# Performance work log

Measured on AMD Instinct MI355X. Metric: run time of the kernel, lower is better.

Reference implementation:

```python
import jax, jax.numpy as jnp
import numpy as np

HIDDEN, N_HEADS, N_KV, HD = 2560, 32, 8, 80
B, S = 2, 2048

def apply_rope(x, cos_f, sin_f):
    # x: [B, S, H, hd]; cos_f/sin_f: [S, hd]
    seq_len = x.shape[1]
    cos = cos_f[:seq_len][None, :, None, :]
    sin = sin_f[:seq_len][None, :, None, :]
    hd = x.shape[-1]
    x1, x2 = x[..., : hd // 2], x[..., hd // 2 :]
    return x * cos + jnp.concatenate([-x2, x1], axis=-1) * sin


def setup_inputs() -> dict:
    key = jax.random.key(0)
    ks = jax.random.split(key, 7)
    sd = 0.02
    return {
        "x": jax.random.normal(ks[0], (B, S, HIDDEN), dtype=jnp.float32),
        "cos_f": jax.random.uniform(ks[1], (S, HD), dtype=jnp.float32),
        "sin_f": jax.random.uniform(ks[2], (S, HD), dtype=jnp.float32),
        "Wq": jax.random.normal(ks[3], (HIDDEN, N_HEADS * HD), dtype=jnp.float32) * sd,
        "Wk": jax.random.normal(ks[4], (HIDDEN, N_KV * HD), dtype=jnp.float32) * sd,
        "Wv": jax.random.normal(ks[5], (HIDDEN, N_KV * HD), dtype=jnp.float32) * sd,
        "Wo": jax.random.normal(ks[6], (N_HEADS * HD, HIDDEN), dtype=jnp.float32) * sd,
    }


def reference(x, cos_f, sin_f, Wq, Wk, Wv, Wo):
    b, s, _ = x.shape
    q = (x @ Wq).reshape(b, s, N_HEADS, HD)
    k = (x @ Wk).reshape(b, s, N_KV, HD)
    v = (x @ Wv).reshape(b, s, N_KV, HD)
    q = apply_rope(q, cos_f, sin_f)
    k = apply_rope(k, cos_f, sin_f)
    g = N_HEADS // N_KV
    k = jnp.repeat(k, g, axis=2)  # [b, s, n_heads, hd]
    v = jnp.repeat(v, g, axis=2)
    q, k, v = [jnp.transpose(t, (0, 2, 1, 3)) for t in (q, k, v)]  # [b, h, s, hd]
    scale = jnp.sqrt(jnp.float32(HD))
    w = jnp.einsum("bhqd,bhkd->bhqk", q, k) / scale
    causal = jnp.triu(jnp.full((s, s), -1e9, dtype=w.dtype), k=1)
    w = w + causal[None, None]
    w = jax.nn.softmax(w.astype(jnp.float32), axis=-1).astype(q.dtype)
    o = jnp.einsum("bhqk,bhkd->bhqd", w, v)
    o = jnp.transpose(o, (0, 2, 1, 3)).reshape(b, s, N_HEADS * HD)
    return o @ Wo
```

## Files before the change

### kernel.cpp

```cpp
#include <hip/hip_runtime.h>
#include <hip/hip_bf16.h>
#include <math.h>

#define HIDDEN 2560
#define NH 32
#define NKV 8
#define HD 80
#define BATCH 2
#define SEQ 2048
#define QH_COLS (NH*HD)
#define KV_COLS (NKV*HD)
#define ROWS (BATCH*SEQ)

typedef __attribute__((ext_vector_type(4))) float floatx4;
typedef __attribute__((ext_vector_type(16))) float floatx16;
typedef __attribute__((ext_vector_type(8))) short shortx8;
typedef __attribute__((ext_vector_type(4))) unsigned short u16x4;
typedef unsigned short u16;

__device__ inline u16 f2bf(float f) { __hip_bfloat16 h = __float2bfloat16(f); return *(u16*)&h; }
__device__ inline int swz(int r) { return (r + (r >> 2)) & 3; }
__device__ inline void storeC(float v, float* p) { *p = v; }
__device__ inline void storeC(float v, u16* p) { *p = f2bf(v); }

#if __has_builtin(__builtin_amdgcn_exp2f)
__device__ inline float fexp2(float x) { return __builtin_amdgcn_exp2f(x); }
#else
__device__ inline float fexp2(float x) { return __expf(x * 0.6931471805599453f); }
#endif

__device__ __forceinline__ unsigned cvtpk(float lo, float hi2) {
    unsigned r;
    asm("v_cvt_pk_bf16_f32 %0, %1, %2" : "=v"(r) : "v"(lo), "v"(hi2));
    return r;
}
__device__ __forceinline__ void pl32swap(unsigned &a, unsigned &b) {
#if __has_builtin(__builtin_amdgcn_permlane32_swap)
    auto r = __builtin_amdgcn_permlane32_swap(a, b, false, false);
    a = r[0]; b = r[1];
#else
    asm("v_permlane32_swap_b32 %0, %1" : "+v"(a), "+v"(b));
#endif
}

__global__ __launch_bounds__(256) void conv_bf16(const float* __restrict__ x,
                                                 u16* __restrict__ y) {
    int i = (blockIdx.x * 256 + threadIdx.x) * 4;
    float4 v = *(const float4*)(x + i);
    u16x4 o = { f2bf(v.x), f2bf(v.y), f2bf(v.z), f2bf(v.w) };
    *(u16x4*)(y + i) = o;
}

__global__ __launch_bounds__(256) void transpose_conv(const float* __restrict__ W,
                                                      u16* __restrict__ Wt,
                                                      int K, int N) {
    __shared__ float tile[64][65];
    const int tid = threadIdx.x;
    const int n0 = blockIdx.x * 64, k0 = blockIdx.y * 64;
    const int r = tid >> 4, c4 = (tid & 15) * 4;
#pragma unroll
    for (int i = 0; i < 4; i++) {
        float4 v = *(const float4*)(W + (size_t)(k0 + r + i * 16) * N + n0 + c4);
        tile[r + i * 16][c4 + 0] = v.x;
        tile[r + i * 16][c4 + 1] = v.y;
        tile[r + i * 16][c4 + 2] = v.z;
        tile[r + i * 16][c4 + 3] = v.w;
    }
    __syncthreads();
    const int n = tid >> 2, kg = (tid & 3) * 16;
    __align__(16) u16 tmp[16];
#pragma unroll
    for (int j = 0; j < 16; j++) tmp[j] = f2bf(tile[kg + j][n]);
    u16* dst = Wt + (size_t)(n0 + n) * K + k0 + kg;
    *(uint4*)dst = *(const uint4*)tmp;
    *(uint4*)(dst + 8) = *(const uint4*)(tmp + 8);
}

template <typename OutT>
__global__ __launch_bounds__(256) void gemm_mfma(const u16* __restrict__ A,
                                                 const u16* __restrict__ Bt,
                                                 OutT* __restrict__ C,
                                                 int M, int N, int K) {
    __shared__ __align__(16) u16 As[128 * 32];
    __shared__ __align__(16) u16 Bs[128 * 32];
    const int tid = threadIdx.x;
    const int wave = tid >> 6, lane = tid & 63;
    const int m16 = lane & 15, quad = lane >> 4;
    const int wr = wave >> 1, wc = wave & 1;
    const int bm = blockIdx.y * 128, bn = blockIdx.x * 128;

    const u16* gA[2]; const u16* gB[2]; u16* lA[2]; u16* lB[2];
#pragma unroll
    for (int i = 0; i < 2; i++) {
        int c = wave + i * 4;
        int o = c * 1024 + lane * 16;
        int r = o >> 6;
        int s = (o >> 4) & 3;
        int kb = s ^ swz(r);
        gA[i] = A  + (size_t)(bm + r) * K + kb * 8;
        gB[i] = Bt + (size_t)(bn + r) * K + kb * 8;
        lA[i] = As + (o >> 1);
        lB[i] = Bs + (o >> 1);
    }
    int offA[4], offB[4];
#pragma unroll
    for (int i = 0; i < 4; i++) {
        int ra = wr * 64 + i * 16 + m16;
        offA[i] = ra * 32 + (quad ^ swz(ra)) * 8;
        int rb = wc * 64 + i * 16 + m16;
        offB[i] = rb * 32 + (quad ^ swz(rb)) * 8;
    }

    floatx4 acc[4][4];
#pragma unroll
    for (int i = 0; i < 4; i++)
#pragma unroll
        for (int j = 0; j < 4; j++) acc[i][j] = (floatx4){0.f, 0.f, 0.f, 0.f};

    for (int k0 = 0; k0 < K; k0 += 32) {
#pragma unroll
        for (int i = 0; i < 2; i++) {
            __builtin_amdgcn_global_load_lds(
                (const __attribute__((address_space(1))) unsigned int*)(gA[i] + k0),
                (__attribute__((address_space(3))) unsigned int*)lA[i], 16, 0, 0);
            __builtin_amdgcn_global_load_lds(
                (const __attribute__((address_space(1))) unsigned int*)(gB[i] + k0),
                (__attribute__((address_space(3))) unsigned int*)lB[i], 16, 0, 0);
        }
        __syncthreads();
        shortx8 af[4], bfr[4];
#pragma unroll
        for (int i = 0; i < 4; i++) af[i] = *(const shortx8*)(As + offA[i]);
#pragma unroll
        for (int j = 0; j < 4; j++) bfr[j] = *(const shortx8*)(Bs + offB[j]);
#pragma unroll
        for (int i = 0; i < 4; i++)
#pragma unroll
            for (int j = 0; j < 4; j++)
                acc[i][j] = __builtin_amdgcn_mfma_f32_16x16x32_bf16(af[i], bfr[j], acc[i][j], 0, 0, 0);
        __syncthreads();
    }
#pragma unroll
    for (int i = 0; i < 4; i++)
#pragma unroll
        for (int j = 0; j < 4; j++)
#pragma unroll
            for (int p = 0; p < 4; p++) {
                int row = bm + wr * 64 + i * 16 + quad * 4 + p;
                int col = bn + wc * 64 + j * 16 + m16;
                storeC(acc[i][j][p], &C[(size_t)row * N + col]);
            }
}

__global__ __launch_bounds__(256) void rope_bf16(__hip_bfloat16* __restrict__ qh,
                                                 __hip_bfloat16* __restrict__ kh,
                                                 const float* __restrict__ cf,
                                                 const float* __restrict__ sf) {
    int idx = blockIdx.x * 256 + threadIdx.x;
    int d  = idx % 40;
    int t  = idx / 40;
    int hh = t % (NH + NKV);
    int g  = t / (NH + NKV);
    int s  = g & (SEQ - 1);
    float c1 = cf[s * HD + d],      s1 = sf[s * HD + d];
    float c2 = cf[s * HD + d + 40], s2 = sf[s * HD + d + 40];
    const float qsc = (hh < NH) ? (float)(0.11180339887498949 * 1.4426950408889634) : 1.0f;
    __hip_bfloat16* p = (hh < NH) ? (qh + (size_t)g * QH_COLS + hh * HD)
                                  : (kh + (size_t)g * KV_COLS + (hh - NH) * HD);
    float x1 = __bfloat162float(p[d]);
    float x2 = __bfloat162float(p[d + 40]);
    p[d]      = __float2bfloat16((x1 * c1 - x2 * s1) * qsc);
    p[d + 40] = __float2bfloat16((x2 * c2 + x1 * s2) * qsc);
}

__device__ __forceinline__ void stage_K(const u16* kg, u16* dst, int wave, int lane) {
#pragma unroll
    for (int t = 0; t < 2; t++) {
        int s = t * 256 + wave * 64 + lane;
        int db = t * 4 + wave;
        __builtin_amdgcn_global_load_lds(
            (const __attribute__((address_space(1))) unsigned int*)(kg + (size_t)lane * KV_COLS + db * 8),
            (__attribute__((address_space(3))) unsigned int*)(dst + s * 8), 16, 0, 0);
    }
    if (wave < 2) {
        int s = 512 + wave * 64 + lane;
        int db = 8 + wave;
        __builtin_amdgcn_global_load_lds(
            (const __attribute__((address_space(1))) unsigned int*)(kg + (size_t)lane * KV_COLS + db * 8),
            (__attribute__((address_space(3))) unsigned int*)(dst + s * 8), 16, 0, 0);
    }
}

__device__ __forceinline__ void load_V(const u16* vg, shortx8* vr, int wave, int lane) {
#pragma unroll
    for (int t = 0; t < 2; t++) {
        int db = t * 4 + wave;
        vr[t] = *(const shortx8*)(vg + (size_t)lane * KV_COLS + db * 8);
    }
    if (wave < 2) vr[2] = *(const shortx8*)(vg + (size_t)lane * KV_COLS + (8 + wave) * 8);
}

__device__ __forceinline__ void scatter_V(u16* Vs, const shortx8* vr, int wave, int lane) {
    const int kc = lane >> 3, jj = lane & 7;
    u16* base = Vs + kc * 768 + jj;
#pragma unroll
    for (int t = 0; t < 2; t++) {
        int db = t * 4 + wave;
#pragma unroll
        for (int i = 0; i < 8; i++) base[db * 64 + ((i ^ kc) << 3)] = vr[t][i];
    }
    if (wave < 2) {
        int db = 8 + wave;
#pragma unroll
        for (int i = 0; i < 8; i++) base[db * 64 + ((i ^ kc) << 3)] = vr[2][i];
    }
}

__global__ __launch_bounds__(256, 3) void attn_mfma(const u16* __restrict__ qg,
                                                    const u16* __restrict__ kgp,
                                                    const u16* __restrict__ vgp,
                                                    u16* __restrict__ ob) {
    __shared__ __align__(16) u16 SM[16384];
    u16* Kbuf = SM;
    u16* Vs   = SM + 10240;

    const int tid  = threadIdx.x;
    const int wave = tid >> 6;
    const int lane = tid & 63;
    const int l31  = lane & 31;
    const int hi   = lane >> 5;

    const int idx = blockIdx.x;
    const int qt  = 15 - (idx >> 6);
    const int hb  = idx & 63;
    const int h   = hb >> 1;
    const int b   = hb & 1;
    const int kvh = h >> 2;
    const int qb  = qt * 128 + wave * 32;

    const u16* qgb = qg + (size_t)(b * SEQ + qt * 128) * QH_COLS + h * HD;
    const u16* kg0 = kgp + (size_t)(b * SEQ) * KV_COLS + kvh * HD;
    const u16* vg0 = vgp + (size_t)(b * SEQ) * KV_COLS + kvh * HD;

    {
        int kc = tid >> 5, o = (tid & 31) * 4;
        *(u16x4*)(Vs + kc * 768 + 640 + o) = (u16x4){0, 0, 0, 0};
    }

#pragma unroll
    for (int t = 0; t < 5; t++) {
        int s = t * 256 + tid;
        int row = s / 10, ch = s % 10;
        __builtin_amdgcn_global_load_lds(
            (const __attribute__((address_space(1))) unsigned int*)(qgb + (size_t)row * QH_COLS + ch * 8),
            (__attribute__((address_space(3))) unsigned int*)(SM + s * 8), 16, 0, 0);
    }
    __syncthreads();
    shortx8 qf[5];
    {
        const u16* qrow = SM + (wave * 32 + l31) * 80 + hi * 8;
#pragma unroll
        for (int c = 0; c < 5; c++) qf[c] = *(const shortx8*)(qrow + c * 16);
    }
    __syncthreads();

    int vbase[4];
#pragma unroll
    for (int c = 0; c < 4; c++) {
        int k8 = c * 2 + hi;
        vbase[c] = k8 * 768 + ((l31 & 24) + ((l31 & 7) ^ k8)) * 8;
    }
    const u16* kfp = Kbuf + hi * 512 + l31 * 8;

    stage_K(kg0, Kbuf, wave, lane);
    shortx8 vr[3];
    load_V(vg0, vr, wave, lane);
    __syncthreads();
    scatter_V(Vs, vr, wave, lane);
    __syncthreads();

    floatx16 Oacc[3];
#pragma unroll
    for (int n = 0; n < 3; n++)
#pragma unroll
        for (int r = 0; r < 16; r++) Oacc[n][r] = 0.0f;
    float mrow = -1.0e30f, lrow = 0.0f;
    int cur = 0;
    const int nkt = 2 * qt + 2;

    for (int kt = 0; kt < nkt; kt++) {
        const bool last = (kt == nkt - 1);
        if (!last) {
            const u16* kg = kg0 + (size_t)(kt + 1) * 64 * KV_COLS;
            const u16* vg = vg0 + (size_t)(kt + 1) * 64 * KV_COLS;
            stage_K(kg, Kbuf + (cur ^ 1) * 5120, wave, lane);
            load_V(vg, vr, wave, lane);
        }

        const bool active = (kt * 64 <= qb + 31);
        if (active) {
            const u16* kp = kfp + cur * 5120;
            const bool kr1   = (kt * 64 + 32 <= qb + 31);
            const bool dmask = (kt * 64 + 63 > qb);
            floatx16 S0, S1;
            {
                floatx16 s;
#pragma unroll
                for (int r = 0; r < 16; r++) s[r] = 0.0f;
#pragma unroll
                for (int c = 0; c < 5; c++) {
                    shortx8 kf = *(const shortx8*)(kp + c * 1024);
                    s = __builtin_amdgcn_mfma_f32_32x32x16_bf16(kf, qf[c], s, 0, 0, 0);
                }
                S0 = s;
            }
            if (kr1) {
                floatx16 s;
#pragma unroll
                for (int r = 0; r < 16; r++) s[r] = 0.0f;
#pragma unroll
                for (int c = 0; c < 5; c++) {
                    shortx8 kf = *(const shortx8*)(kp + c * 1024 + 256);
                    s = __builtin_amdgcn_mfma_f32_32x32x16_bf16(kf, qf[c], s, 0, 0, 0);
                }
                S1 = s;
            }
            const int qrel = qb + l31 - kt * 64;
            if (dmask) {
#pragma unroll
                for (int r = 0; r < 16; r++) {
                    int rr = (r & 3) + 8 * (r >> 2) + 4 * hi;
                    if (rr > qrel) S0[r] = -1.0e30f;
                    if (kr1 && (32 + rr) > qrel) S1[r] = -1.0e30f;
                }
            }
            float mx = mrow;
#pragma unroll
            for (int r = 0; r < 16; r++) mx = fmaxf(mx, S0[r]);
            if (kr1) {
#pragma unroll
                for (int r = 0; r < 16; r++) mx = fmaxf(mx, S1[r]);
            }
            mx = fmaxf(mx, __shfl_xor(mx, 32));
            if (!__all(mx - mrow <= 8.0f)) {
                float alpha = fexp2(mrow - mx);
                lrow *= alpha;
#pragma unroll
                for (int n = 0; n < 3; n++)
#pragma unroll
                    for (int r = 0; r < 16; r++) Oacc[n][r] *= alpha;
                mrow = mx;
            }
            float rsum = 0.0f;
#pragma unroll
            for (int r = 0; r < 16; r++) { float p = fexp2(S0[r] - mrow); rsum += p; S0[r] = p; }
            if (kr1) {
#pragma unroll
                for (int r = 0; r < 16; r++) { float p = fexp2(S1[r] - mrow); rsum += p; S1[r] = p; }
            }
            rsum += __shfl_xor(rsum, 32);
            lrow += rsum;

#pragma unroll
            for (int kr = 0; kr < 2; kr++) {
                if (kr == 1 && !kr1) break;
                floatx16& Sv = (kr == 0) ? S0 : S1;
                unsigned d0[4], d1[4];
#pragma unroll
                for (int m = 0; m < 4; m++) {
                    d0[m] = cvtpk(Sv[4 * m + 0], Sv[4 * m + 1]);
                    d1[m] = cvtpk(Sv[4 * m + 2], Sv[4 * m + 3]);
                }
#pragma unroll
                for (int cb = 0; cb < 2; cb++) {
                    int c = kr * 2 + cb;
                    if (kt * 64 + c * 16 > qb + 31) break;
                    unsigned x0 = d0[2 * cb], y0 = d0[2 * cb + 1];
                    unsigned x1 = d1[2 * cb], y1 = d1[2 * cb + 1];
                    pl32swap(x0, y0);
                    pl32swap(x1, y1);
                    union { unsigned u[4]; shortx8 s8; } pf;
                    pf.u[0] = x0; pf.u[1] = x1; pf.u[2] = y0; pf.u[3] = y1;
#pragma unroll
                    for (int n = 0; n < 3; n++) {
                        shortx8 vf = *(const shortx8*)(Vs + vbase[c] + n * 256);
                        Oacc[n] = __builtin_amdgcn_mfma_f32_32x32x16_bf16(vf, pf.s8, Oacc[n], 0, 0, 0);
                    }
                }
            }
        }

        if (last) break;
        __syncthreads();
        scatter_V(Vs, vr, wave, lane);
        cur ^= 1;
        __syncthreads();
    }

    const float invl = 1.0f / lrow;
    u16* op = ob + (size_t)(b * SEQ + qt * 128 + wave * 32 + l31) * QH_COLS + h * HD + 4 * hi;
#pragma unroll
    for (int n = 0; n < 3; n++) {
        const int mmax = (n == 2) ? 2 : 4;
#pragma unroll
        for (int m = 0; m < mmax; m++) {
            u16x4 o4 = { f2bf(Oacc[n][4 * m + 0] * invl), f2bf(Oacc[n][4 * m + 1] * invl),
                         f2bf(Oacc[n][4 * m + 2] * invl), f2bf(Oacc[n][4 * m + 3] * invl) };
            *(u16x4*)(op + n * 32 + 8 * m) = o4;
        }
    }
}

extern "C" void kernel_launch(void* const* d_in, const int* in_sizes, int n_in,
                              void* d_out, int out_size, void* d_ws, size_t ws_size,
                              hipStream_t stream) {
    const float* x    = (const float*)d_in[0];
    const float* cf   = (const float*)d_in[1];
    const float* sf   = (const float*)d_in[2];
    const float* Wq   = (const float*)d_in[3];
    const float* Wk   = (const float*)d_in[4];
    const float* Wv   = (const float*)d_in[5];
    const float* Wo   = (const float*)d_in[6];
    float* out = (float*)d_out;

    u16* xh  = (u16*)d_ws;
    u16* Wqt = xh  + (size_t)ROWS * QH_COLS;
    u16* Wkt = Wqt + (size_t)QH_COLS * HIDDEN;
    u16* Wvt = Wkt + (size_t)KV_COLS * HIDDEN;
    u16* Wot = Wvt + (size_t)KV_COLS * HIDDEN;
    u16* qh  = Wot + (size_t)HIDDEN * QH_COLS;
    u16* kh  = qh  + (size_t)ROWS * QH_COLS;
    u16* vh  = kh  + (size_t)ROWS * KV_COLS;
    u16* obh = xh;

    dim3 blk(256);
    conv_bf16<<<(ROWS * HIDDEN / 4) / 256, blk, 0, stream>>>(x, xh);
    transpose_conv<<<dim3(QH_COLS / 64, HIDDEN / 64), blk, 0, stream>>>(Wq, Wqt, HIDDEN, QH_COLS);
    transpose_conv<<<dim3(KV_COLS / 64, HIDDEN / 64), blk, 0, stream>>>(Wk, Wkt, HIDDEN, KV_COLS);
    transpose_conv<<<dim3(KV_COLS / 64, HIDDEN / 64), blk, 0, stream>>>(Wv, Wvt, HIDDEN, KV_COLS);
    transpose_conv<<<dim3(HIDDEN / 64, QH_COLS / 64), blk, 0, stream>>>(Wo, Wot, QH_COLS, HIDDEN);

    gemm_mfma<u16><<<dim3(QH_COLS / 128, ROWS / 128), blk, 0, stream>>>(xh, Wqt, qh, ROWS, QH_COLS, HIDDEN);
    gemm_mfma<u16><<<dim3(KV_COLS / 128, ROWS / 128), blk, 0, stream>>>(xh, Wkt, kh, ROWS, KV_COLS, HIDDEN);
    gemm_mfma<u16><<<dim3(KV_COLS / 128, ROWS / 128), blk, 0, stream>>>(xh, Wvt, vh, ROWS, KV_COLS, HIDDEN);

    rope_bf16<<<(ROWS * (NH + NKV) * 40) / 256, blk, 0, stream>>>((__hip_bfloat16*)qh, (__hip_bfloat16*)kh, cf, sf);
    attn_mfma<<<dim3(16 * 64), blk, 0, stream>>>(qh, kh, vh, obh);

    gemm_mfma<float><<<dim3(HIDDEN / 128, ROWS / 128), blk, 0, stream>>>(obh, Wot, out, ROWS, HIDDEN, QH_COLS);
}
```

Baseline: 549.9 us.

## Fuse QKV projections into one GEMM and use 256x256 pipelined MFMA tiles

Concatenates the Wq, Wk and Wv transposed weights so a single GEMM writes an interleaved QKV buffer. RoPE and attention are updated to read it with the wider row stride. The GEMM is replaced with a 512-thread, 256x256-tile kernel with 64-wide K steps, double-buffered global_load_lds prefetch two stages ahead, split barriers and setprio around MFMA bursts. The goal is fewer launches, more data reuse per tile and better overlap of loads with matrix math. The costs are much more LDS per block (128 KB), fewer blocks for the small output projection grid (10x16), and a strided QKV layout for attention loads.

```diff
diff --git a/kernel.cpp b/kernel.cpp
--- a/kernel.cpp
+++ b/kernel.cpp
@@ -10,6 +10,7 @@
 #define SEQ 2048
 #define QH_COLS (NH*HD)
 #define KV_COLS (NKV*HD)
+#define QKV_COLS (QH_COLS + 2*KV_COLS)
 #define ROWS (BATCH*SEQ)
 
 typedef __attribute__((ext_vector_type(4))) float floatx4;
@@ -19,7 +20,6 @@
 typedef unsigned short u16;
 
 __device__ inline u16 f2bf(float f) { __hip_bfloat16 h = __float2bfloat16(f); return *(u16*)&h; }
-__device__ inline int swz(int r) { return (r + (r >> 2)) & 3; }
 __device__ inline void storeC(float v, float* p) { *p = v; }
 __device__ inline void storeC(float v, u16* p) { *p = f2bf(v); }
 
@@ -43,6 +43,10 @@
 #endif
 }
 
+#define GLL(gp, lp) __builtin_amdgcn_global_load_lds( \
+    (const __attribute__((address_space(1))) unsigned int*)(gp), \
+    (__attribute__((address_space(3))) unsigned int*)(lp), 16, 0, 0)
+
 __global__ __launch_bounds__(256) void conv_bf16(const float* __restrict__ x,
                                                  u16* __restrict__ y) {
     int i = (blockIdx.x * 256 + threadIdx.x) * 4;
@@ -77,83 +81,124 @@
 }
 
 template <typename OutT>
-__global__ __launch_bounds__(256) void gemm_mfma(const u16* __restrict__ A,
-                                                 const u16* __restrict__ Bt,
-                                                 OutT* __restrict__ C,
-                                                 int M, int N, int K) {
-    __shared__ __align__(16) u16 As[128 * 32];
-    __shared__ __align__(16) u16 Bs[128 * 32];
+__global__ __launch_bounds__(512, 2) void gemm256(const u16* __restrict__ A,
+                                                  const u16* __restrict__ Bt,
+                                                  OutT* __restrict__ C,
+                                                  int M, int N, int K) {
+    __shared__ __align__(16) u16 SM[65536];
     const int tid = threadIdx.x;
     const int wave = tid >> 6, lane = tid & 63;
     const int m16 = lane & 15, quad = lane >> 4;
-    const int wr = wave >> 1, wc = wave & 1;
-    const int bm = blockIdx.y * 128, bn = blockIdx.x * 128;
-
-    const u16* gA[2]; const u16* gB[2]; u16* lA[2]; u16* lB[2];
-#pragma unroll
-    for (int i = 0; i < 2; i++) {
-        int c = wave + i * 4;
-        int o = c * 1024 + lane * 16;
-        int r = o >> 6;
-        int s = (o >> 4) & 3;
-        int kb = s ^ swz(r);
-        gA[i] = A  + (size_t)(bm + r) * K + kb * 8;
-        gB[i] = Bt + (size_t)(bn + r) * K + kb * 8;
-        lA[i] = As + (o >> 1);
-        lB[i] = Bs + (o >> 1);
-    }
-    int offA[4], offB[4];
-#pragma unroll
-    for (int i = 0; i < 4; i++) {
-        int ra = wr * 64 + i * 16 + m16;
-        offA[i] = ra * 32 + (quad ^ swz(ra)) * 8;
-        int rb = wc * 64 + i * 16 + m16;
-        offB[i] = rb * 32 + (quad ^ swz(rb)) * 8;
-    }
-
-    floatx4 acc[4][4];
-#pragma unroll
-    for (int i = 0; i < 4; i++)
+    const int wm = wave >> 2, wn = wave & 3;
+    const int bm = blockIdx.y * 256, bn = blockIdx.x * 256;
+
+    const int srow = (wave & 3) * 64 + lane;
+    const int skc  = wave >> 2;
+    const u16* pA = A  + (size_t)(bm + srow) * K + skc * 8;
+    const u16* pB = Bt + (size_t)(bn + srow) * K + skc * 8;
+    u16* lsA = SM + skc * 2048 + (wave & 3) * 512 + lane * 8;
+    u16* lsB = lsA + 32768;
+
+    const int aoff = quad * 2048 + (wm * 128 + m16) * 8;
+    const int boff = quad * 2048 + (wn * 64 + m16) * 8 + 32768;
+
+    floatx4 acc[8][4];
+#pragma unroll
+    for (int i = 0; i < 8; i++)
 #pragma unroll
         for (int j = 0; j < 4; j++) acc[i][j] = (floatx4){0.f, 0.f, 0.f, 0.f};
 
-    for (int k0 = 0; k0 < K; k0 += 32) {
-#pragma unroll
-        for (int i = 0; i < 2; i++) {
-            __builtin_amdgcn_global_load_lds(
-                (const __attribute__((address_space(1))) unsigned int*)(gA[i] + k0),
-                (__attribute__((address_space(3))) unsigned int*)lA[i], 16, 0, 0);
-            __builtin_amdgcn_global_load_lds(
-                (const __attribute__((address_space(1))) unsigned int*)(gB[i] + k0),
-                (__attribute__((address_space(3))) unsigned int*)lB[i], 16, 0, 0);
-        }
-        __syncthreads();
-        shortx8 af[4], bfr[4];
-#pragma unroll
-        for (int i = 0; i < 4; i++) af[i] = *(const shortx8*)(As + offA[i]);
-#pragma unroll
-        for (int j = 0; j < 4; j++) bfr[j] = *(const shortx8*)(Bs + offB[j]);
-#pragma unroll
-        for (int i = 0; i < 4; i++)
-#pragma unroll
-            for (int j = 0; j < 4; j++)
-                acc[i][j] = __builtin_amdgcn_mfma_f32_16x16x32_bf16(af[i], bfr[j], acc[i][j], 0, 0, 0);
-        __syncthreads();
-    }
-#pragma unroll
-    for (int i = 0; i < 4; i++)
+    const int nkt = K >> 6;
+
+#pragma unroll
+    for (int t = 0; t < 2; t++) {
+        const int tb = t * 16384, tc = t * 64;
+        GLL(pA + tc,      lsA + tb);        GLL(pA + tc + 16, lsA + tb + 4096);
+        GLL(pB + tc,      lsB + tb);        GLL(pB + tc + 16, lsB + tb + 4096);
+        GLL(pA + tc + 32, lsA + tb + 8192); GLL(pA + tc + 48, lsA + tb + 12288);
+        GLL(pB + tc + 32, lsB + tb + 8192); GLL(pB + tc + 48, lsB + tb + 12288);
+    }
+    asm volatile("s_waitcnt vmcnt(8)" ::: "memory");
+    __builtin_amdgcn_s_barrier();
+
+    for (int kt = 0; kt < nkt; ++kt) {
+        const int ab = (kt & 1) * 16384;
+        const bool pf = (kt + 2 < nkt);
+        const int pc = (kt + 2) * 64;
+        shortx8 af[8], b0, b1, b2, b3;
+
+#pragma unroll
+        for (int i = 0; i < 8; i++) af[i] = *(const shortx8*)(SM + ab + aoff + i * 128);
+        b0 = *(const shortx8*)(SM + ab + boff);
+        b1 = *(const shortx8*)(SM + ab + boff + 128);
+        if (pf) { GLL(pA + pc, lsA + ab); GLL(pA + pc + 16, lsA + ab + 4096); }
+        __builtin_amdgcn_s_barrier();
+        __builtin_amdgcn_s_setprio(1);
+#pragma unroll
+        for (int i = 0; i < 8; i++) {
+            acc[i][0] = __builtin_amdgcn_mfma_f32_16x16x32_bf16(af[i], b0, acc[i][0], 0, 0, 0);
+            acc[i][1] = __builtin_amdgcn_mfma_f32_16x16x32_bf16(af[i], b1, acc[i][1], 0, 0, 0);
+        }
+        __builtin_amdgcn_s_setprio(0);
+        __builtin_amdgcn_s_barrier();
+
+        b2 = *(const shortx8*)(SM + ab + boff + 256);
+        b3 = *(const shortx8*)(SM + ab + boff + 384);
+        if (pf) { GLL(pB + pc, lsB + ab); GLL(pB + pc + 16, lsB + ab + 4096); }
+        __builtin_amdgcn_s_barrier();
+        __builtin_amdgcn_s_setprio(1);
+#pragma unroll
+        for (int i = 0; i < 8; i++) {
+            acc[i][2] = __builtin_amdgcn_mfma_f32_16x16x32_bf16(af[i], b2, acc[i][2], 0, 0, 0);
+            acc[i][3] = __builtin_amdgcn_mfma_f32_16x16x32_bf16(af[i], b3, acc[i][3], 0, 0, 0);
+        }
+        __builtin_amdgcn_s_setprio(0);
+        __builtin_amdgcn_s_barrier();
+
+#pragma unroll
+        for (int i = 0; i < 8; i++) af[i] = *(const shortx8*)(SM + ab + 8192 + aoff + i * 128);
+        b0 = *(const shortx8*)(SM + ab + 8192 + boff);
+        b1 = *(const shortx8*)(SM + ab + 8192 + boff + 128);
+        if (pf) { GLL(pA + pc + 32, lsA + ab + 8192); GLL(pA + pc + 48, lsA + ab + 12288); }
+        __builtin_amdgcn_s_barrier();
+        __builtin_amdgcn_s_setprio(1);
+#pragma unroll
+        for (int i = 0; i < 8; i++) {
+            acc[i][0] = __builtin_amdgcn_mfma_f32_16x16x32_bf16(af[i], b0, acc[i][0], 0, 0, 0);
+            acc[i][1] = __builtin_amdgcn_mfma_f32_16x16x32_bf16(af[i], b1, acc[i][1], 0, 0, 0);
+        }
+        __builtin_amdgcn_s_setprio(0);
+        __builtin_amdgcn_s_barrier();
+
+        b2 = *(const shortx8*)(SM + ab + 8192 + boff + 256);
+        b3 = *(const shortx8*)(SM + ab + 8192 + boff + 384);
+        if (pf) { GLL(pB + pc + 32, lsB + ab + 8192); GLL(pB + pc + 48, lsB + ab + 12288); }
+        __builtin_amdgcn_s_barrier();
+        __builtin_amdgcn_s_setprio(1);
+#pragma unroll
+        for (int i = 0; i < 8; i++) {
+            acc[i][2] = __builtin_amdgcn_mfma_f32_16x16x32_bf16(af[i], b2, acc[i][2], 0, 0, 0);
+            acc[i][3] = __builtin_amdgcn_mfma_f32_16x16x32_bf16(af[i], b3, acc[i][3], 0, 0, 0);
+        }
+        __builtin_amdgcn_s_setprio(0);
+        if (pf) asm volatile("s_waitcnt vmcnt(8)" ::: "memory");
+        else    asm volatile("s_waitcnt vmcnt(0)" ::: "memory");
+        __builtin_amdgcn_s_barrier();
+    }
+
+#pragma unroll
+    for (int i = 0; i < 8; i++)
 #pragma unroll
         for (int j = 0; j < 4; j++)
 #pragma unroll
             for (int p = 0; p < 4; p++) {
-                int row = bm + wr * 64 + i * 16 + quad * 4 + p;
-                int col = bn + wc * 64 + j * 16 + m16;
+                int row = bm + wm * 128 + i * 16 + quad * 4 + p;
+                int col = bn + wn * 64 + j * 16 + m16;
                 storeC(acc[i][j][p], &C[(size_t)row * N + col]);
             }
 }
 
-__global__ __launch_bounds__(256) void rope_bf16(__hip_bfloat16* __restrict__ qh,
-                                                 __hip_bfloat16* __restrict__ kh,
+__global__ __launch_bounds__(256) void rope_bf16(__hip_bfloat16* __restrict__ qkv,
                                                  const float* __restrict__ cf,
                                                  const float* __restrict__ sf) {
     int idx = blockIdx.x * 256 + threadIdx.x;
@@ -165,8 +210,8 @@
     float c1 = cf[s * HD + d],      s1 = sf[s * HD + d];
     float c2 = cf[s * HD + d + 40], s2 = sf[s * HD + d + 40];
     const float qsc = (hh < NH) ? (float)(0.11180339887498949 * 1.4426950408889634) : 1.0f;
-    __hip_bfloat16* p = (hh < NH) ? (qh + (size_t)g * QH_COLS + hh * HD)
-                                  : (kh + (size_t)g * KV_COLS + (hh - NH) * HD);
+    __hip_bfloat16* p = (hh < NH) ? (qkv + (size_t)g * QKV_COLS + hh * HD)
+                                  : (qkv + (size_t)g * QKV_COLS + QH_COLS + (hh - NH) * HD);
     float x1 = __bfloat162float(p[d]);
     float x2 = __bfloat162float(p[d + 40]);
     p[d]      = __float2bfloat16((x1 * c1 - x2 * s1) * qsc);
@@ -178,16 +223,12 @@
     for (int t = 0; t < 2; t++) {
         int s = t * 256 + wave * 64 + lane;
         int db = t * 4 + wave;
-        __builtin_amdgcn_global_load_lds(
-            (const __attribute__((address_space(1))) unsigned int*)(kg + (size_t)lane * KV_COLS + db * 8),
-            (__attribute__((address_space(3))) unsigned int*)(dst + s * 8), 16, 0, 0);
+        GLL(kg + (size_t)lane * QKV_COLS + db * 8, dst + s * 8);
     }
     if (wave < 2) {
         int s = 512 + wave * 64 + lane;
         int db = 8 + wave;
-        __builtin_amdgcn_global_load_lds(
-            (const __attribute__((address_space(1))) unsigned int*)(kg + (size_t)lane * KV_COLS + db * 8),
-            (__attribute__((address_space(3))) unsigned int*)(dst + s * 8), 16, 0, 0);
+        GLL(kg + (size_t)lane * QKV_COLS + db * 8, dst + s * 8);
     }
 }
 
@@ -195,9 +236,9 @@
 #pragma unroll
     for (int t = 0; t < 2; t++) {
         int db = t * 4 + wave;
-        vr[t] = *(const shortx8*)(vg + (size_t)lane * KV_COLS + db * 8);
-    }
-    if (wave < 2) vr[2] = *(const shortx8*)(vg + (size_t)lane * KV_COLS + (8 + wave) * 8);
+        vr[t] = *(const shortx8*)(vg + (size_t)lane * QKV_COLS + db * 8);
+    }
+    if (wave < 2) vr[2] = *(const shortx8*)(vg + (size_t)lane * QKV_COLS + (8 + wave) * 8);
 }
 
 __device__ __forceinline__ void scatter_V(u16* Vs, const shortx8* vr, int wave, int lane) {
@@ -216,9 +257,7 @@
     }
 }
 
-__global__ __launch_bounds__(256, 3) void attn_mfma(const u16* __restrict__ qg,
-                                                    const u16* __restrict__ kgp,
-                                                    const u16* __restrict__ vgp,
+__global__ __launch_bounds__(256, 3) void attn_mfma(const u16* __restrict__ qkv,
                                                     u16* __restrict__ ob) {
     __shared__ __align__(16) u16 SM[16384];
     u16* Kbuf = SM;
@@ -238,9 +277,9 @@
     const int kvh = h >> 2;
     const int qb  = qt * 128 + wave * 32;
 
-    const u16* qgb = qg + (size_t)(b * SEQ + qt * 128) * QH_COLS + h * HD;
-    const u16* kg0 = kgp + (size_t)(b * SEQ) * KV_COLS + kvh * HD;
-    const u16* vg0 = vgp + (size_t)(b * SEQ) * KV_COLS + kvh * HD;
+    const u16* qgb = qkv + (size_t)(b * SEQ + qt * 128) * QKV_COLS + h * HD;
+    const u16* kg0 = qkv + (size_t)(b * SEQ) * QKV_COLS + QH_COLS + kvh * HD;
+    const u16* vg0 = qkv + (size_t)(b * SEQ) * QKV_COLS + QH_COLS + KV_COLS + kvh * HD;
 
     {
         int kc = tid >> 5, o = (tid & 31) * 4;
@@ -251,9 +290,7 @@
     for (int t = 0; t < 5; t++) {
         int s = t * 256 + tid;
         int row = s / 10, ch = s % 10;
-        __builtin_amdgcn_global_load_lds(
-            (const __attribute__((address_space(1))) unsigned int*)(qgb + (size_t)row * QH_COLS + ch * 8),
-            (__attribute__((address_space(3))) unsigned int*)(SM + s * 8), 16, 0, 0);
+        GLL(qgb + (size_t)row * QKV_COLS + ch * 8, SM + s * 8);
     }
     __syncthreads();
     shortx8 qf[5];
@@ -291,8 +328,8 @@
     for (int kt = 0; kt < nkt; kt++) {
         const bool last = (kt == nkt - 1);
         if (!last) {
-            const u16* kg = kg0 + (size_t)(kt + 1) * 64 * KV_COLS;
-            const u16* vg = vg0 + (size_t)(kt + 1) * 64 * KV_COLS;
+            const u16* kg = kg0 + (size_t)(kt + 1) * 64 * QKV_COLS;
+            const u16* vg = vg0 + (size_t)(kt + 1) * 64 * QKV_COLS;
             stage_K(kg, Kbuf + (cur ^ 1) * 5120, wave, lane);
             load_V(vg, vr, wave, lane);
         }
@@ -423,29 +460,23 @@
     const float* Wo   = (const float*)d_in[6];
     float* out = (float*)d_out;
 
-    u16* xh  = (u16*)d_ws;
-    u16* Wqt = xh  + (size_t)ROWS * QH_COLS;
-    u16* Wkt = Wqt + (size_t)QH_COLS * HIDDEN;
-    u16* Wvt = Wkt + (size_t)KV_COLS * HIDDEN;
-    u16* Wot = Wvt + (size_t)KV_COLS * HIDDEN;
-    u16* qh  = Wot + (size_t)HIDDEN * QH_COLS;
-    u16* kh  = qh  + (size_t)ROWS * QH_COLS;
-    u16* vh  = kh  + (size_t)ROWS * KV_COLS;
-    u16* obh = xh;
+    u16* xh    = (u16*)d_ws;
+    u16* Wqkvt = xh    + (size_t)ROWS * HIDDEN;
+    u16* Wot   = Wqkvt + (size_t)QKV_COLS * HIDDEN;
+    u16* qkv   = Wot   + (size_t)QH_COLS * HIDDEN;
+    u16* obh   = xh;
 
     dim3 blk(256);
     conv_bf16<<<(ROWS * HIDDEN / 4) / 256, blk, 0, stream>>>(x, xh);
-    transpose_conv<<<dim3(QH_COLS / 64, HIDDEN / 64), blk, 0, stream>>>(Wq, Wqt, HIDDEN, QH_COLS);
-    transpose_conv<<<dim3(KV_COLS / 64, HIDDEN / 64), blk, 0, stream>>>(Wk, Wkt, HIDDEN, KV_COLS);
-    transpose_conv<<<dim3(KV_COLS / 64, HIDDEN / 64), blk, 0, stream>>>(Wv, Wvt, HIDDEN, KV_COLS);
+    transpose_conv<<<dim3(QH_COLS / 64, HIDDEN / 64), blk, 0, stream>>>(Wq, Wqkvt, HIDDEN, QH_COLS);
+    transpose_conv<<<dim3(KV_COLS / 64, HIDDEN / 64), blk, 0, stream>>>(Wk, Wqkvt + (size_t)QH_COLS * HIDDEN, HIDDEN, KV_COLS);
+    transpose_conv<<<dim3(KV_COLS / 64, HIDDEN / 64), blk, 0, stream>>>(Wv, Wqkvt + (size_t)(QH_COLS + KV_COLS) * HIDDEN, HIDDEN, KV_COLS);
     transpose_conv<<<dim3(HIDDEN / 64, QH_COLS / 64), blk, 0, stream>>>(Wo, Wot, QH_COLS, HIDDEN);
 
-    gemm_mfma<u16><<<dim3(QH_COLS / 128, ROWS / 128), blk, 0, stream>>>(xh, Wqt, qh, ROWS, QH_COLS, HIDDEN);
-    gemm_mfma<u16><<<dim3(KV_COLS / 128, ROWS / 128), blk, 0, stream>>>(xh, Wkt, kh, ROWS, KV_COLS, HIDDEN);
-    gemm_mfma<u16><<<dim3(KV_COLS / 128, ROWS / 128), blk, 0, stream>>>(xh, Wvt, vh, ROWS, KV_COLS, HIDDEN);
-
-    rope_bf16<<<(ROWS * (NH + NKV) * 40) / 256, blk, 0, stream>>>((__hip_bfloat16*)qh, (__hip_bfloat16*)kh, cf, sf);
-    attn_mfma<<<dim3(16 * 64), blk, 0, stream>>>(qh, kh, vh, obh);
-
-    gemm_mfma<float><<<dim3(HIDDEN / 128, ROWS / 128), blk, 0, stream>>>(obh, Wot, out, ROWS, HIDDEN, QH_COLS);
-}
+    gemm256<u16><<<dim3(QKV_COLS / 256, ROWS / 256), dim3(512), 0, stream>>>(xh, Wqkvt, qkv, ROWS, QKV_COLS, HIDDEN);
+
+    rope_bf16<<<(ROWS * (NH + NKV) * 40) / 256, blk, 0, stream>>>((__hip_bfloat16*)qkv, cf, sf);
+    attn_mfma<<<dim3(16 * 64), blk, 0, stream>>>(qkv, obh);
+
+    gemm256<float><<<dim3(HIDDEN / 256, ROWS / 256), dim3(512), 0, stream>>>(obh, Wot, out, ROWS, HIDDEN, QH_COLS);
+}
```

Result: faster. 479.9 us (-12.7%).
